# Kernel tuning notes

Hardware: AMD Instinct MI355X
Metric: run time of the kernel (lower is better)

Reference implementation:

```python
import jax, jax.numpy as jnp
import numpy as np

B, S, DM = 2, 2048, 2048
H, DH = 16, 128
EPS = 1e-6


def rmsnorm(t, w):
    # normalize over last dim (head_dim), fp32 math
    var = jnp.mean(jnp.square(t), axis=-1, keepdims=True)
    return t * jax.lax.rsqrt(var + EPS) * w


def apply_rope(t, freqs):
    # t: (B,S,H,D); freqs: (S,1,D/2,2,2)
    b, s, h, d = t.shape
    t2 = t.reshape(b, s, h, 2, d // 2)
    t2 = jnp.moveaxis(t2, -2, -1)[..., None, :]  # (B,S,H,D/2,1,2)
    out = freqs[..., 0] * t2[..., 0] + freqs[..., 1] * t2[..., 1]  # (B,S,H,D/2,2)
    out = jnp.moveaxis(out, -1, -2).reshape(b, s, h, d)
    return out.astype(t.dtype)


def setup_inputs() -> dict:
    key = jax.random.key(0)
    ks = jax.random.split(key, 6)
    sc = 0.02
    return {
        "x": jax.random.normal(ks[0], (B, S, DM), jnp.float32),
        "rope_emb": jax.random.normal(ks[1], (S, 1, DH // 2, 2, 2), jnp.float32),
        "wq": jax.random.normal(ks[2], (DM, DM), jnp.float32) * sc,
        "wk": jax.random.normal(ks[3], (DM, DM), jnp.float32) * sc,
        "wv": jax.random.normal(ks[4], (DM, DM), jnp.float32) * sc,
        "wo": jax.random.normal(ks[5], (DM, DM), jnp.float32) * sc,
        "q_norm_w": jnp.ones((DH,), jnp.float32),
        "k_norm_w": jnp.ones((DH,), jnp.float32),
    }


def reference(x, rope_emb, wq, wk, wv, wo, q_norm_w, k_norm_w):
    b, s, _ = x.shape
    q = (x @ wq.T).reshape(b, s, H, DH)
    k = (x @ wk.T).reshape(b, s, H, DH)
    v = (x @ wv.T).reshape(b, s, H, DH)
    q = rmsnorm(q, q_norm_w)
    k = rmsnorm(k, k_norm_w)
    q = apply_rope(q, rope_emb)
    k = apply_rope(k, rope_emb)
    scale = 1.0 / np.sqrt(DH).astype(np.float32)
    scores = jnp.einsum('bqhd,bkhd->bhqk', q, k) * scale
    attn = jax.nn.softmax(scores, axis=-1)
    out = jnp.einsum('bhqk,bkhd->bqhd', attn, v).reshape(b, s, H * DH)
    return out @ wo.T
```

## Files before the change

### kernel.cpp

```cpp
#include <hip/hip_runtime.h>

typedef __bf16 bf16x8 __attribute__((ext_vector_type(8)));
typedef __bf16 bf16x4 __attribute__((ext_vector_type(4)));
typedef float floatx4 __attribute__((ext_vector_type(4)));

#define GK 2048
#define S_LEN 2048
#define NH 16
#define DH 128
#define NKT (GK / 64)

__device__ __forceinline__ void gl2lds16c(const __bf16* g, char* l) {
    __builtin_amdgcn_global_load_lds(
        (const __attribute__((address_space(1))) void*)g,
        (__attribute__((address_space(3))) void*)l, 16, 0, 0);
}

__global__ __launch_bounds__(256) void cvt_bf16(const float* __restrict__ in,
                                                __bf16* __restrict__ out, int n4) {
    int i = blockIdx.x * 256 + threadIdx.x;
    if (i < n4) {
        const float4 v = ((const float4*)in)[i];
        bf16x4 h;
        h[0] = (__bf16)v.x; h[1] = (__bf16)v.y; h[2] = (__bf16)v.z; h[3] = (__bf16)v.w;
        ((bf16x4*)out)[i] = h;
    }
}

__global__ __launch_bounds__(256) void cvt3_bf16(const float* __restrict__ a,
                                                 const float* __restrict__ b,
                                                 const float* __restrict__ c,
                                                 __bf16* __restrict__ out) {
    const int per = 2048 * 2048 / 4;
    int i = blockIdx.x * 256 + threadIdx.x;
    const float* src = a; int j = i;
    if (i >= 2 * per)      { src = c; j = i - 2 * per; }
    else if (i >= per)     { src = b; j = i - per; }
    const float4 v = ((const float4*)src)[j];
    bf16x4 h;
    h[0] = (__bf16)v.x; h[1] = (__bf16)v.y; h[2] = (__bf16)v.z; h[3] = (__bf16)v.w;
    ((bf16x4*)out)[i] = h;
}

__device__ __forceinline__ int xcd_remap(int L, int nwg) {
    return (L & 7) * (nwg >> 3) + (L >> 3);
}

__device__ __forceinline__ void gemm_body4(const __bf16* __restrict__ A,
                                           const __bf16* __restrict__ W,
                                           int m0, int n0, char* lds,
                                           floatx4 (*acc)[4]) {
    const int t = threadIdx.x, l = t & 63, wave = t >> 6;
    const int fr = l & 15, fq = l >> 4;
    const int wm = wave >> 2, wn = wave & 3;

    const int swcol = ((l & 7) * 8) ^ (((l >> 3) & 7) * 8);
    const __bf16* gA = A + (size_t)(m0 + wave * 8 + (l >> 3)) * GK + swcol;
    const __bf16* gW = W + (size_t)(n0 + wave * 8 + (l >> 3)) * GK + swcol;
    char* const ldsW = lds + wave * 1024;

    auto stageA = [&](int p, int kt, int c) {
        gl2lds16c(gA + (size_t)c * 64 * GK + kt * 64,
                  ldsW + p * 49152 + c * 8192);
    };
    auto stageBh = [&](int p, int kt, int h) {
        gl2lds16c(gW + (size_t)h * 64 * GK + kt * 64,
                  ldsW + p * 49152 + 16384 + h * 8192);
    };

    stageA(0, 0, 0); stageA(0, 0, 1);
#pragma unroll
    for (int h = 0; h < 4; h++) stageBh(0, 0, h);
    stageA(1, 1, 0); stageA(1, 1, 1);
#pragma unroll
    for (int h = 0; h < 4; h++) stageBh(1, 1, h);

    const int sw = (fr & 7) << 4;
    const int cb0 = (fq * 16) ^ sw;
    const int cb1 = (64 + fq * 16) ^ sw;

    for (int t0 = 0; t0 < NKT; t0++) {
        const int p = t0 & 1;
        if (t0 == NKT - 1) { asm volatile("s_waitcnt vmcnt(0)" ::: "memory"); }
        else               { asm volatile("s_waitcnt vmcnt(6)" ::: "memory"); }
        __builtin_amdgcn_s_barrier();
        asm volatile("" ::: "memory");

        const char* bufA = lds + p * 49152;
        const char* bufB = bufA + 16384;

        bf16x8 bB[4][2];
#pragma unroll
        for (int j = 0; j < 4; j++) {
            const char* rb = bufB + (wn * 64 + j * 16 + fr) * 128;
            bB[j][0] = *(const bf16x8*)(rb + cb0);
            bB[j][1] = *(const bf16x8*)(rb + cb1);
        }
        bf16x8 af[2][2];
        {
            const char* ra = bufA + (wm * 16 + fr) * 128;
            af[0][0] = *(const bf16x8*)(ra + cb0);
            af[0][1] = *(const bf16x8*)(ra + cb1);
        }

#pragma unroll
        for (int q = 0; q < 4; q++) {
            if (t0 + 2 < NKT) {
                if (q == 1) { stageBh(p, t0 + 2, 0); stageBh(p, t0 + 2, 1); }
                if (q == 2) { stageBh(p, t0 + 2, 2); stageBh(p, t0 + 2, 3); stageA(p, t0 + 2, 0); }
            }
            if (q < 3) {
                const char* ra = bufA + ((q + 1) * 32 + wm * 16 + fr) * 128;
                af[(q + 1) & 1][0] = *(const bf16x8*)(ra + cb0);
                af[(q + 1) & 1][1] = *(const bf16x8*)(ra + cb1);
            }
            __builtin_amdgcn_s_setprio(1);
#pragma unroll
            for (int j = 0; j < 4; j++) {
                acc[q][j] = __builtin_amdgcn_mfma_f32_16x16x32_bf16(af[q & 1][0], bB[j][0], acc[q][j], 0, 0, 0);
                acc[q][j] = __builtin_amdgcn_mfma_f32_16x16x32_bf16(af[q & 1][1], bB[j][1], acc[q][j], 0, 0, 0);
            }
            __builtin_amdgcn_s_setprio(0);
            __builtin_amdgcn_s_barrier();
            asm volatile("" ::: "memory");
        }
        if (t0 + 2 < NKT) stageA(p, t0 + 2, 1);
    }
}

__global__ __launch_bounds__(512, 2) void gemm_qkv(const __bf16* __restrict__ A,
                                                   const __bf16* __restrict__ W,
                                                   __bf16* __restrict__ qb,
                                                   __bf16* __restrict__ kb,
                                                   __bf16* __restrict__ vbT) {
    extern __shared__ __align__(16) char lds[];
    const int gx = gridDim.x;
    const int L = blockIdx.x + gx * blockIdx.y;
    const int tid2 = xcd_remap(L, gx * (int)gridDim.y);
    const int m0 = (tid2 / gx) * 128, n0 = (tid2 % gx) * 256;
    floatx4 acc[4][4] = {};
    gemm_body4(A, W, m0, n0, lds, acc);

    const int lane = threadIdx.x & 63, wave = threadIdx.x >> 6;
    const int fr = lane & 15, fq = lane >> 4;
    const int wm = wave >> 2, wn = wave & 3;
    const int which = n0 >> 11;
    const int nc0 = n0 & 2047;

    for (int mi = 0; mi < 4; mi++)
        for (int j = 0; j < 4; j++) {
            const int row = m0 + mi * 32 + wm * 16 + fq * 4;
            const int col = nc0 + wn * 64 + j * 16 + fr;
            if (which == 2) {
                __bf16* Cp = vbT + (((size_t)(row & ~2047)) << 11) +
                             (size_t)col * 2048 + (row & 2047);
                bf16x4 hv;
                for (int r = 0; r < 4; r++) hv[r] = (__bf16)acc[mi][j][r];
                *(bf16x4*)Cp = hv;
            } else {
                __bf16* dst = which ? kb : qb;
                for (int r = 0; r < 4; r++)
                    dst[(size_t)(row + r) * 2048 + col] = (__bf16)acc[mi][j][r];
            }
        }
}

__global__ __launch_bounds__(512, 2) void gemm_out(const __bf16* __restrict__ A,
                                                   const __bf16* __restrict__ W,
                                                   float* __restrict__ C) {
    extern __shared__ __align__(16) char lds[];
    const int gx = gridDim.x;
    const int L = blockIdx.x + gx * blockIdx.y;
    const int tid2 = xcd_remap(L, gx * (int)gridDim.y);
    const int m0 = (tid2 / gx) * 128, n0 = (tid2 % gx) * 256;
    floatx4 acc[4][4] = {};
    gemm_body4(A, W, m0, n0, lds, acc);

    const int lane = threadIdx.x & 63, wave = threadIdx.x >> 6;
    const int fr = lane & 15, fq = lane >> 4;
    const int wm = wave >> 2, wn = wave & 3;
    for (int mi = 0; mi < 4; mi++)
        for (int j = 0; j < 4; j++) {
            const int row = m0 + mi * 32 + wm * 16 + fq * 4;
            const int col = n0 + wn * 64 + j * 16 + fr;
            for (int r = 0; r < 4; r++)
                C[(size_t)(row + r) * 2048 + col] = acc[mi][j][r];
        }
}

__global__ __launch_bounds__(256) void rmsrope(__bf16* __restrict__ qb,
                                               __bf16* __restrict__ kb,
                                               const float* __restrict__ rope,
                                               const float* __restrict__ qw,
                                               const float* __restrict__ kw) {
    const int lane = threadIdx.x & 63;
    const int row = blockIdx.x * 4 + (threadIdx.x >> 6);
    __bf16* p = (blockIdx.y ? kb : qb) + (size_t)row * DH;
    const float* w = blockIdx.y ? kw : qw;
    const int s = (row >> 4) & (S_LEN - 1);

    float t0 = (float)p[lane];
    float t1 = (float)p[lane + 64];
    float ss = t0 * t0 + t1 * t1;
    for (int o = 32; o; o >>= 1) ss += __shfl_xor(ss, o, 64);
    const float inv = rsqrtf(ss * (1.0f / 128.0f) + 1e-6f);
    t0 *= inv * w[lane];
    t1 *= inv * w[lane + 64];

    const float4 f = *(const float4*)(rope + (size_t)s * 256 + lane * 4);
    p[lane]      = (__bf16)(f.x * t0 + f.y * t1);
    p[lane + 64] = (__bf16)(f.z * t0 + f.w * t1);
}

__global__ __launch_bounds__(256, 2) void flash(const __bf16* __restrict__ Q,
                                                const __bf16* __restrict__ K,
                                                const __bf16* __restrict__ Vt_g,
                                                __bf16* __restrict__ O) {
    extern __shared__ __align__(16) char lds[];

    const int t = threadIdx.x, lane = t & 63, wave = t >> 6;
    const int fr = lane & 15, fq = lane >> 4;

    const int n = blockIdx.x + (int)gridDim.x * blockIdx.y;
    const int by = (n & 7) * 4 + (n >> 7);
    const int bx = (n >> 3) & 15;
    const int b = by >> 4, h = by & 15;

    const size_t baseQ = (size_t)b * S_LEN * 2048 + h * 128;
    const size_t baseV = (size_t)b * 2048 * 2048 + (size_t)h * 128 * 2048;
    const int q0 = bx * 128 + wave * 32;
    const float sc2 = 0.08838834764831845f * 1.4426950408889634f;
    const float M2 = 12.0f * 1.4426950408889634f;

    bf16x8 qf[2][4];
#pragma unroll
    for (int i2 = 0; i2 < 2; i2++) {
        const __bf16* qp = Q + baseQ + (size_t)(q0 + i2 * 16 + fr) * 2048 + fq * 8;
#pragma unroll
        for (int c = 0; c < 4; c++) qf[i2][c] = *(const bf16x8*)(qp + c * 32);
    }
    asm volatile("s_waitcnt vmcnt(0)" ::: "memory");

    bf16x8 onesb;
#pragma unroll
    for (int e = 0; e < 8; e++) onesb[e] = (__bf16)1.0f;

    const int l4 = lane >> 4;
    const int c16 = lane & 15;
    const int l3 = lane >> 3;
    const int c8 = lane & 7;
    const __bf16* gK0 = K + baseQ + (size_t)(wave * 16 + l4) * 2048 + (c16 ^ l4) * 8;
    const __bf16* gK1 = K + baseQ + (size_t)(wave * 16 + l4) * 2048 + (c16 ^ (4 + l4)) * 8;
    const __bf16* gV  = Vt_g + baseV + (size_t)(wave * 8 + l3) * 2048 + (c8 ^ l3) * 8;

    char* const kdw = lds + wave * 4096;
    char* const vdw = lds + 32768 + wave * 1024;

    auto stage = [&](int p, int it2) {
        const size_t ko = (size_t)it2 * 64 * 2048;
        char* kd = kdw + p * 16384;
        gl2lds16c(gK0 + ko,                      kd);
        gl2lds16c(gK1 + ko + (size_t)4 * 2048,   kd + 1024);
        gl2lds16c(gK0 + ko + (size_t)8 * 2048,   kd + 2048);
        gl2lds16c(gK1 + ko + (size_t)12 * 2048,  kd + 3072);
        const __bf16* v = gV + it2 * 64;
        char* vd = vdw + p * 16384;
        gl2lds16c(v,                        vd);
        gl2lds16c(v + (size_t)32 * 2048,    vd + 4096);
        gl2lds16c(v + (size_t)64 * 2048,    vd + 8192);
        gl2lds16c(v + (size_t)96 * 2048,    vd + 12288);
    };

    stage(0, 0);
    stage(1, 1);

    floatx4 oa[2][9] = {};
    char* const Pw = lds + 65536 + wave * 4096;
    const int sw = (fr & 7) << 4;

    for (int it = 0; it < 32; ++it) {
        const int p = it & 1;
        if (it == 31) { asm volatile("s_waitcnt vmcnt(0)" ::: "memory"); }
        else          { asm volatile("s_waitcnt vmcnt(8)" ::: "memory"); }
        __builtin_amdgcn_s_barrier();
        asm volatile("" ::: "memory");

        const char* Kb = lds + p * 16384;
        const char* Vb = lds + 32768 + p * 16384;

        floatx4 sacc[2][4] = {};
#pragma unroll
        for (int j = 0; j < 4; j++) {
            const char* kr = Kb + (j * 16 + fr) * 256;
            const bf16x8 kf0 = *(const bf16x8*)(kr + ((0 + fq * 16) ^ sw));
            const bf16x8 kf1 = *(const bf16x8*)(kr + ((64 + fq * 16) ^ sw));
            const bf16x8 kf2 = *(const bf16x8*)(kr + ((128 + fq * 16) ^ sw));
            const bf16x8 kf3 = *(const bf16x8*)(kr + ((192 + fq * 16) ^ sw));
            __builtin_amdgcn_s_setprio(1);
            sacc[0][j] = __builtin_amdgcn_mfma_f32_16x16x32_bf16(qf[0][0], kf0, sacc[0][j], 0, 0, 0);
            sacc[1][j] = __builtin_amdgcn_mfma_f32_16x16x32_bf16(qf[1][0], kf0, sacc[1][j], 0, 0, 0);
            sacc[0][j] = __builtin_amdgcn_mfma_f32_16x16x32_bf16(qf[0][1], kf1, sacc[0][j], 0, 0, 0);
            sacc[1][j] = __builtin_amdgcn_mfma_f32_16x16x32_bf16(qf[1][1], kf1, sacc[1][j], 0, 0, 0);
            sacc[0][j] = __builtin_amdgcn_mfma_f32_16x16x32_bf16(qf[0][2], kf2, sacc[0][j], 0, 0, 0);
            sacc[1][j] = __builtin_amdgcn_mfma_f32_16x16x32_bf16(qf[1][2], kf2, sacc[1][j], 0, 0, 0);
            sacc[0][j] = __builtin_amdgcn_mfma_f32_16x16x32_bf16(qf[0][3], kf3, sacc[0][j], 0, 0, 0);
            sacc[1][j] = __builtin_amdgcn_mfma_f32_16x16x32_bf16(qf[1][3], kf3, sacc[1][j], 0, 0, 0);
            __builtin_amdgcn_s_setprio(0);
        }

#pragma unroll
        for (int i2 = 0; i2 < 2; i2++)
#pragma unroll
            for (int r = 0; r < 4; r++) {
                const int row = i2 * 16 + fq * 4 + r;
                char* pr = Pw + row * 128;
                const int rsw = ((fq * 4 + r) & 7) << 4;
#pragma unroll
                for (int j = 0; j < 4; j++)
                    *(__bf16*)(pr + ((j * 32 + fr * 2) ^ rsw)) =
                        (__bf16)exp2f(fmaf(sc2, sacc[i2][j][r], -M2));
            }

        bf16x8 pf[2][2];
#pragma unroll
        for (int i2 = 0; i2 < 2; i2++) {
            const char* pr = Pw + (i2 * 16 + fr) * 128;
            pf[i2][0] = *(const bf16x8*)(pr + ((fq * 16) ^ sw));
            pf[i2][1] = *(const bf16x8*)(pr + ((64 + fq * 16) ^ sw));
        }
#pragma unroll
        for (int nb = 0; nb < 8; nb++) {
            const char* vr = Vb + (nb * 16 + fr) * 128;
            const bf16x8 vf0 = *(const bf16x8*)(vr + ((fq * 16) ^ sw));
            const bf16x8 vf1 = *(const bf16x8*)(vr + ((64 + fq * 16) ^ sw));
            __builtin_amdgcn_s_setprio(1);
            oa[0][nb] = __builtin_amdgcn_mfma_f32_16x16x32_bf16(pf[0][0], vf0, oa[0][nb], 0, 0, 0);
            oa[1][nb] = __builtin_amdgcn_mfma_f32_16x16x32_bf16(pf[1][0], vf0, oa[1][nb], 0, 0, 0);
            oa[0][nb] = __builtin_amdgcn_mfma_f32_16x16x32_bf16(pf[0][1], vf1, oa[0][nb], 0, 0, 0);
            oa[1][nb] = __builtin_amdgcn_mfma_f32_16x16x32_bf16(pf[1][1], vf1, oa[1][nb], 0, 0, 0);
            __builtin_amdgcn_s_setprio(0);
        }
        oa[0][8] = __builtin_amdgcn_mfma_f32_16x16x32_bf16(pf[0][0], onesb, oa[0][8], 0, 0, 0);
        oa[1][8] = __builtin_amdgcn_mfma_f32_16x16x32_bf16(pf[1][0], onesb, oa[1][8], 0, 0, 0);
        oa[0][8] = __builtin_amdgcn_mfma_f32_16x16x32_bf16(pf[0][1], onesb, oa[0][8], 0, 0, 0);
        oa[1][8] = __builtin_amdgcn_mfma_f32_16x16x32_bf16(pf[1][1], onesb, oa[1][8], 0, 0, 0);

        __builtin_amdgcn_s_barrier();
        asm volatile("" ::: "memory");
        if (it < 30) stage(p, it + 2);
    }

    for (int i2 = 0; i2 < 2; i2++)
        for (int r = 0; r < 4; r++) {
            const float inv = 1.0f / oa[i2][8][r];
            __bf16* op = O + baseQ + (size_t)(q0 + i2 * 16 + fq * 4 + r) * 2048;
            for (int nb = 0; nb < 8; nb++)
                op[nb * 16 + fr] = (__bf16)(oa[i2][nb][r] * inv);
        }
}

extern "C" void kernel_launch(void* const* d_in, const int* in_sizes, int n_in,
                              void* d_out, int out_size, void* d_ws, size_t ws_size,
                              hipStream_t stream) {
    const float* x    = (const float*)d_in[0];
    const float* rope = (const float*)d_in[1];
    const float* wq   = (const float*)d_in[2];
    const float* wk   = (const float*)d_in[3];
    const float* wv   = (const float*)d_in[4];
    const float* wo   = (const float*)d_in[5];
    const float* qnw  = (const float*)d_in[6];
    const float* knw  = (const float*)d_in[7];
    float* out = (float*)d_out;

    static bool attr_set = false;
    if (!attr_set) {
        hipFuncSetAttribute((const void*)gemm_qkv,
                            hipFuncAttributeMaxDynamicSharedMemorySize, 98304);
        hipFuncSetAttribute((const void*)gemm_out,
                            hipFuncAttributeMaxDynamicSharedMemorySize, 98304);
        hipFuncSetAttribute((const void*)flash,
                            hipFuncAttributeMaxDynamicSharedMemorySize, 81920);
        attr_set = true;
    }

    const size_t NTOK = 2 * 2048;
    const size_t ELEMS = NTOK * 2048;
    __bf16* xb  = (__bf16*)d_ws;
    __bf16* qb  = xb + ELEMS;
    __bf16* kb  = qb + ELEMS;
    __bf16* vbT = kb + ELEMS;
    __bf16* ob  = xb;
    __bf16* wqkv = (__bf16*)d_out;
    __bf16* wob  = qb;

    cvt_bf16<<<(int)(ELEMS / 4) / 256, 256, 0, stream>>>(x, xb, (int)(ELEMS / 4));
    cvt3_bf16<<<3 * (2048 * 2048 / 4) / 256, 256, 0, stream>>>(wq, wk, wv, wqkv);
    gemm_qkv<<<dim3(6144 / 256, (unsigned)(NTOK / 128)), 512, 98304, stream>>>(xb, wqkv, qb, kb, vbT);
    rmsrope<<<dim3((unsigned)(NTOK * 16 / 4), 2), 256, 0, stream>>>(qb, kb, rope, qnw, knw);
    flash<<<dim3(S_LEN / 128, 2 * 16), 256, 81920, stream>>>(qb, kb, vbT, ob);
    cvt_bf16<<<(int)(2048 * 2048 / 4) / 256, 256, 0, stream>>>(wo, wob, 2048 * 2048 / 4);
    gemm_out<<<dim3(2048 / 256, (unsigned)(NTOK / 128)), 512, 98304, stream>>>(ob, wob, out);
}
```

Before: 406.6 us.

## Retile QKV GEMM to 256x192 blocks with a new pipelined body

Adds a new GEMM main loop that computes 256x192 output tiles instead of 128x256. Each block now stages four A sub-tiles and three W sub-tiles per K step into a larger double-buffered LDS area of 112 KB. The aim is more arithmetic per loaded byte and a grid of 512 blocks (32x16) instead of 768. The epilogue now picks the q/k/v destination per 16-column fragment, because a 192-wide tile can straddle a q/k/v boundary. The larger LDS footprint per block, together with 512 threads at two blocks per CU, may cut occupancy.

```diff
diff --git a/kernel.cpp b/kernel.cpp
--- a/kernel.cpp
+++ b/kernel.cpp
@@ -46,6 +46,99 @@
     return (L & 7) * (nwg >> 3) + (L >> 3);
 }
 
+__device__ __forceinline__ void gemm_body5(const __bf16* __restrict__ A,
+                                           const __bf16* __restrict__ W,
+                                           int m0, int n0, char* lds,
+                                           floatx4 (*acc)[3]) {
+    const int t = threadIdx.x, l = t & 63, wave = t >> 6;
+    const int fr = l & 15, fq = l >> 4;
+    const int wm = wave >> 2, wn = wave & 3;
+
+    const int swcol = ((l & 7) * 8) ^ (((l >> 3) & 7) * 8);
+    const __bf16* gA = A + (size_t)(m0 + wave * 8 + (l >> 3)) * GK + swcol;
+    const __bf16* gW = W + (size_t)(n0 + wave * 8 + (l >> 3)) * GK + swcol;
+    char* const ldsW = lds + wave * 1024;
+
+    auto stageA = [&](int p, int kt, int q) {
+        gl2lds16c(gA + (size_t)q * 64 * GK + kt * 64,
+                  ldsW + p * 57344 + q * 8192);
+    };
+    auto stageBh = [&](int p, int kt, int h) {
+        gl2lds16c(gW + (size_t)h * 64 * GK + kt * 64,
+                  ldsW + p * 57344 + 32768 + h * 8192);
+    };
+
+#pragma unroll
+    for (int q = 0; q < 4; q++) stageA(0, 0, q);
+#pragma unroll
+    for (int h = 0; h < 3; h++) stageBh(0, 0, h);
+#pragma unroll
+    for (int q = 0; q < 4; q++) stageA(1, 1, q);
+#pragma unroll
+    for (int h = 0; h < 3; h++) stageBh(1, 1, h);
+
+    const int sw = (fr & 7) << 4;
+    const int cb0 = (fq * 16) ^ sw;
+    const int cb1 = (64 + fq * 16) ^ sw;
+
+    for (int t0 = 0; t0 < NKT; t0++) {
+        const int p = t0 & 1;
+        if (t0 == NKT - 1) { asm volatile("s_waitcnt vmcnt(0)" ::: "memory"); }
+        else               { asm volatile("s_waitcnt vmcnt(7)" ::: "memory"); }
+        __builtin_amdgcn_s_barrier();
+        asm volatile("" ::: "memory");
+
+        const char* bufA = lds + p * 57344;
+        const char* bufB = bufA + 32768;
+
+        bf16x8 bB[3][2];
+#pragma unroll
+        for (int j = 0; j < 3; j++) {
+            const char* rb = bufB + (wn * 48 + j * 16 + fr) * 128;
+            bB[j][0] = *(const bf16x8*)(rb + cb0);
+            bB[j][1] = *(const bf16x8*)(rb + cb1);
+        }
+        bf16x8 af[2][2][2];
+        {
+            const char* ra = bufA + (wm * 32 + fr) * 128;
+#pragma unroll
+            for (int i = 0; i < 2; i++) {
+                af[0][i][0] = *(const bf16x8*)(ra + i * 2048 + cb0);
+                af[0][i][1] = *(const bf16x8*)(ra + i * 2048 + cb1);
+            }
+        }
+
+#pragma unroll
+        for (int q = 0; q < 4; q++) {
+            if (t0 + 2 < NKT) {
+                if (q == 1) { stageA(p, t0 + 2, 0); stageBh(p, t0 + 2, 0); stageBh(p, t0 + 2, 1); }
+                if (q == 2) { stageA(p, t0 + 2, 1); stageBh(p, t0 + 2, 2); }
+                if (q == 3) { stageA(p, t0 + 2, 2); }
+            }
+            if (q < 3) {
+                const char* ra = bufA + ((q + 1) * 64 + wm * 32 + fr) * 128;
+#pragma unroll
+                for (int i = 0; i < 2; i++) {
+                    af[(q + 1) & 1][i][0] = *(const bf16x8*)(ra + i * 2048 + cb0);
+                    af[(q + 1) & 1][i][1] = *(const bf16x8*)(ra + i * 2048 + cb1);
+                }
+            }
+            __builtin_amdgcn_s_setprio(1);
+#pragma unroll
+            for (int i = 0; i < 2; i++)
+#pragma unroll
+                for (int j = 0; j < 3; j++) {
+                    acc[2 * q + i][j] = __builtin_amdgcn_mfma_f32_16x16x32_bf16(af[q & 1][i][0], bB[j][0], acc[2 * q + i][j], 0, 0, 0);
+                    acc[2 * q + i][j] = __builtin_amdgcn_mfma_f32_16x16x32_bf16(af[q & 1][i][1], bB[j][1], acc[2 * q + i][j], 0, 0, 0);
+                }
+            __builtin_amdgcn_s_setprio(0);
+            __builtin_amdgcn_s_barrier();
+            asm volatile("" ::: "memory");
+        }
+        if (t0 + 2 < NKT) stageA(p, t0 + 2, 3);
+    }
+}
+
 __device__ __forceinline__ void gemm_body4(const __bf16* __restrict__ A,
                                            const __bf16* __restrict__ W,
                                            int m0, int n0, char* lds,
@@ -137,20 +230,20 @@
     const int gx = gridDim.x;
     const int L = blockIdx.x + gx * blockIdx.y;
     const int tid2 = xcd_remap(L, gx * (int)gridDim.y);
-    const int m0 = (tid2 / gx) * 128, n0 = (tid2 % gx) * 256;
-    floatx4 acc[4][4] = {};
-    gemm_body4(A, W, m0, n0, lds, acc);
+    const int m0 = (tid2 / gx) * 256, n0 = (tid2 % gx) * 192;
+    floatx4 acc[8][3] = {};
+    gemm_body5(A, W, m0, n0, lds, acc);
 
     const int lane = threadIdx.x & 63, wave = threadIdx.x >> 6;
     const int fr = lane & 15, fq = lane >> 4;
     const int wm = wave >> 2, wn = wave & 3;
-    const int which = n0 >> 11;
-    const int nc0 = n0 & 2047;
-
-    for (int mi = 0; mi < 4; mi++)
-        for (int j = 0; j < 4; j++) {
-            const int row = m0 + mi * 32 + wm * 16 + fq * 4;
-            const int col = nc0 + wn * 64 + j * 16 + fr;
+
+    for (int mi = 0; mi < 8; mi++)
+        for (int j = 0; j < 3; j++) {
+            const int row = m0 + (mi >> 1) * 64 + wm * 32 + (mi & 1) * 16 + fq * 4;
+            const int c0 = n0 + wn * 48 + j * 16;
+            const int which = c0 >> 11;
+            const int col = (c0 & 2047) + fr;
             if (which == 2) {
                 __bf16* Cp = vbT + (((size_t)(row & ~2047)) << 11) +
                              (size_t)col * 2048 + (row & 2047);
@@ -375,7 +468,7 @@
     static bool attr_set = false;
     if (!attr_set) {
         hipFuncSetAttribute((const void*)gemm_qkv,
-                            hipFuncAttributeMaxDynamicSharedMemorySize, 98304);
+                            hipFuncAttributeMaxDynamicSharedMemorySize, 114688);
         hipFuncSetAttribute((const void*)gemm_out,
                             hipFuncAttributeMaxDynamicSharedMemorySize, 98304);
         hipFuncSetAttribute((const void*)flash,
@@ -395,7 +488,7 @@
 
     cvt_bf16<<<(int)(ELEMS / 4) / 256, 256, 0, stream>>>(x, xb, (int)(ELEMS / 4));
     cvt3_bf16<<<3 * (2048 * 2048 / 4) / 256, 256, 0, stream>>>(wq, wk, wv, wqkv);
-    gemm_qkv<<<dim3(6144 / 256, (unsigned)(NTOK / 128)), 512, 98304, stream>>>(xb, wqkv, qb, kb, vbT);
+    gemm_qkv<<<dim3(6144 / 192, (unsigned)(NTOK / 256)), 512, 114688, stream>>>(xb, wqkv, qb, kb, vbT);
     rmsrope<<<dim3((unsigned)(NTOK * 16 / 4), 2), 256, 0, stream>>>(qb, kb, rope, qnw, knw);
     flash<<<dim3(S_LEN / 128, 2 * 16), 256, 81920, stream>>>(qb, kb, vbT, ob);
     cvt_bf16<<<(int)(2048 * 2048 / 4) / 256, 256, 0, stream>>>(wo, wob, 2048 * 2048 / 4);
```

After: 420.5 us. +3.4%, slower.
